# Optimization experiments

Measured on AMD Instinct MI355X. Metric: run time of the kernel, lower is better.

The kernel has to match this reference:

```python
import jax, jax.numpy as jnp
import numpy as np

C = 256
CLS_DIM = 512
GROUPS = C // 4
EPS = 1e-5


def group_norm(x, w, b, groups=GROUPS, eps=EPS):
    # x: [N, C, H, W]
    N, Cc, H, W = x.shape
    xg = x.reshape(N, groups, Cc // groups, H, W)
    mu = xg.mean(axis=(2, 3, 4), keepdims=True)
    var = xg.var(axis=(2, 3, 4), keepdims=True)
    xn = ((xg - mu) * jax.lax.rsqrt(var + eps)).reshape(N, Cc, H, W)
    return xn * w[None, :, None, None] + b[None, :, None, None]


def setup_inputs() -> dict:
    key = jax.random.key(0)
    ks = jax.random.split(key, 12)
    N, H, W = 32, 64, 64
    s = 0.02
    return {
        "X": jax.random.normal(ks[0], (N, C, H, W), jnp.float32),
        "cls": jax.random.normal(ks[1], (N, CLS_DIM), jnp.float32),
        "ln_w": 1.0 + s * jax.random.normal(ks[2], (C,), jnp.float32),
        "ln_b": s * jax.random.normal(ks[3], (C,), jnp.float32),
        "wq": jax.random.normal(ks[4], (C, CLS_DIM), jnp.float32) / np.sqrt(CLS_DIM),
        "bq": s * jax.random.normal(ks[5], (C,), jnp.float32),
        "wk": jax.random.normal(ks[6], (C, CLS_DIM), jnp.float32) / np.sqrt(CLS_DIM),
        "bk": s * jax.random.normal(ks[7], (C,), jnp.float32),
        "conv_w": jax.random.normal(ks[8], (C, C), jnp.float32) / np.sqrt(C),
        "conv_b": s * jax.random.normal(ks[9], (C,), jnp.float32),
        "gn_w": 1.0 + s * jax.random.normal(ks[10], (C,), jnp.float32),
        "gn_b": s * jax.random.normal(ks[11], (C,), jnp.float32),
    }


def reference(X, cls, ln_w, ln_b, wq, bq, wk, bk, conv_w, conv_b, gn_w, gn_b):
    res = X
    Xn = group_norm(X, ln_w, ln_b)
    # NOTE: original code swaps names: K <- Q_emb(cls), Q <- K_emb(cls)
    K = jax.nn.elu(cls @ wq.T + bq) + 1.0              # [N, C]
    Q = (jax.nn.elu(cls @ wk.T + bk) + 1.0) / jnp.sqrt(jnp.float32(C))
    # einsum 'nclw,nco->nolw' with o=1: per-pixel channel contraction with K
    s = jnp.einsum("nchw,nc->nhw", Xn, K)              # [N, H, W]
    # einsum 'nolw,nco->nclw': rank-1 outer product with Q
    X2 = s[:, None, :, :] * Q[:, :, None, None]        # [N, C, H, W]
    # 1x1 conv
    Y = jnp.einsum("nchw,oc->nohw", X2, conv_w) + conv_b[None, :, None, None]
    return group_norm(Y, gn_w, gn_b) + res
```

## Files before the change

### kernel.cpp

```cpp
#include <hip/hip_runtime.h>
#include <math.h>

#define EPSV 1e-5f

typedef float f4v __attribute__((ext_vector_type(4)));

__device__ __forceinline__ float waveReduceSum(float v) {
#pragma unroll
    for (int o = 32; o > 0; o >>= 1) v += __shfl_down(v, o, 64);
    return v;
}

__global__ void k_kq(const float* __restrict__ cls,
                     const float* __restrict__ wq, const float* __restrict__ bq,
                     const float* __restrict__ wk, const float* __restrict__ bk,
                     const float* __restrict__ ln_w,
                     float* __restrict__ Kb, float* __restrict__ Qb,
                     float* __restrict__ Kw) {
    int w = blockIdx.x * 4 + (threadIdx.x >> 6);
    int lane = threadIdx.x & 63;
    int n = w >> 8, c = w & 255;
    const float* cp = cls + (size_t)n * 512;
    const float* qp = wq + (size_t)c * 512;
    const float* kp = wk + (size_t)c * 512;
    float aK = 0.f, aQ = 0.f;
#pragma unroll
    for (int i = 0; i < 8; ++i) {
        int kk = lane + i * 64;
        float cv = cp[kk];
        aK += cv * qp[kk];
        aQ += cv * kp[kk];
    }
    aK = waveReduceSum(aK);
    aQ = waveReduceSum(aQ);
    if (lane == 0) {
        float xk = aK + bq[c];
        float xq = aQ + bk[c];
        float Kv = (xk > 0.f ? xk : expf(xk) - 1.f) + 1.f;
        float Qv = ((xq > 0.f ? xq : expf(xq) - 1.f) + 1.f) * 0.0625f;
        Kb[w] = Kv;
        Qb[w] = Qv;
        Kw[w] = Kv * ln_w[c];
    }
}

__global__ void __launch_bounds__(512) k_pass1(
        const float* __restrict__ X, const float* __restrict__ Kw,
        float* __restrict__ W, float* __restrict__ Sp, float* __restrict__ S2p) {
    int n = blockIdx.x >> 4, tile = blockIdx.x & 15;
    int wv = threadIdx.x >> 6, lane = threadIdx.x & 63;
    __shared__ float kws[256];
    if (threadIdx.x < 256) kws[threadIdx.x] = Kw[n * 256 + threadIdx.x];
    __syncthreads();
    int pix = tile * 256 + lane * 4;
    const float* xb = X + ((size_t)n * 256 << 12) + pix;
#pragma unroll
    for (int go = 0; go < 8; ++go) {
        int g = wv * 8 + go;
        int c0 = g * 4;
        float ax = 0.f, ay = 0.f, az = 0.f, aw = 0.f;
        float s = 0.f, s2 = 0.f;
#pragma unroll
        for (int j = 0; j < 4; ++j) {
            float4 v = *(const float4*)(xb + ((size_t)(c0 + j) << 12));
            float kv = kws[c0 + j];
            ax += kv * v.x; ay += kv * v.y; az += kv * v.z; aw += kv * v.w;
            s  += v.x + v.y + v.z + v.w;
            s2 += v.x * v.x + v.y * v.y + v.z * v.z + v.w * v.w;
        }
        float4 acc = {ax, ay, az, aw};
        *(float4*)(W + ((size_t)(n * 64 + g) << 12) + pix) = acc;
        s = waveReduceSum(s);
        s2 = waveReduceSum(s2);
        if (lane == 0) {
            Sp[blockIdx.x * 64 + g] = s;
            S2p[blockIdx.x * 64 + g] = s2;
        }
    }
}

__global__ void k_s(const float* __restrict__ W,
                    const float* __restrict__ Sp, const float* __restrict__ S2p,
                    const float* __restrict__ Kb, const float* __restrict__ Kw,
                    const float* __restrict__ ln_b,
                    float* __restrict__ sbuf,
                    float* __restrict__ p1, float* __restrict__ p2) {
    int n = blockIdx.x >> 2, tile = blockIdx.x & 3;
    int t = threadIdx.x;
    __shared__ float ivs[64];
    __shared__ float Bsh;
    __shared__ float q1[4], q2[4];
    if (t < 64) {
        float S = 0.f, S2 = 0.f;
#pragma unroll
        for (int tl = 0; tl < 16; ++tl) {
            S  += Sp[(n * 16 + tl) * 64 + t];
            S2 += S2p[(n * 16 + tl) * 64 + t];
        }
        float mu = S * (1.f / 16384.f);
        float var = S2 * (1.f / 16384.f) - mu * mu;
        float iv = rsqrtf(var + EPSV);
        ivs[t] = iv;
        float t1 = 0.f, t2 = 0.f;
#pragma unroll
        for (int j = 0; j < 4; ++j) {
            int c = t * 4 + j;
            t1 += Kb[n * 256 + c] * ln_b[c];
            t2 += Kw[n * 256 + c];
        }
        float r = waveReduceSum(t1 - iv * mu * t2);
        if (t == 0) Bsh = r;
    }
    __syncthreads();
    int pix = tile * 1024 + t * 4;
    const float* wb = W + ((size_t)n * 64 << 12) + pix;
    float Bn = Bsh;
    float sx = Bn, sy = Bn, sz = Bn, sw = Bn;
#pragma unroll 8
    for (int g = 0; g < 64; ++g) {
        float4 v = *(const float4*)(wb + ((size_t)g << 12));
        float iv = ivs[g];
        sx += iv * v.x; sy += iv * v.y; sz += iv * v.z; sw += iv * v.w;
    }
    float4 s4 = {sx, sy, sz, sw};
    *(float4*)(sbuf + n * 4096 + pix) = s4;
    float r1 = waveReduceSum(sx + sy + sz + sw);
    float r2 = waveReduceSum(sx * sx + sy * sy + sz * sz + sw * sw);
    int lane = t & 63, wid = t >> 6;
    if (lane == 0) { q1[wid] = r1; q2[wid] = r2; }
    __syncthreads();
    if (t == 0) {
        p1[blockIdx.x] = q1[0] + q1[1] + q1[2] + q1[3];
        p2[blockIdx.x] = q2[0] + q2[1] + q2[2] + q2[3];
    }
}

__global__ void k_ab(const float* __restrict__ p1, const float* __restrict__ p2,
                     const float* __restrict__ Qb, const float* __restrict__ conv_w,
                     const float* __restrict__ conv_b,
                     const float* __restrict__ gn_w, const float* __restrict__ gn_b,
                     float* __restrict__ alpha, float* __restrict__ beta) {
    int n = blockIdx.x, t = threadIdx.x;
    __shared__ float qs[256];
    __shared__ float rs[256];
    __shared__ float Ms1s, Ms2s;
    qs[t] = Qb[n * 256 + t];
    if (t == 0) {
        float a = 0.f, b = 0.f;
#pragma unroll
        for (int i = 0; i < 4; ++i) { a += p1[n * 4 + i]; b += p2[n * 4 + i]; }
        Ms1s = a * (1.f / 4096.f);
        Ms2s = b * (1.f / 4096.f);
    }
    __syncthreads();
    const float4* cw = (const float4*)(conv_w + (size_t)t * 256);
    const float4* q4 = (const float4*)qs;
    float acc = 0.f;
#pragma unroll 8
    for (int k = 0; k < 64; ++k) {
        float4 w4 = cw[k], v4 = q4[k];
        acc += w4.x * v4.x + w4.y * v4.y + w4.z * v4.z + w4.w * v4.w;
    }
    rs[t] = acc;
    __syncthreads();
    float Ms1 = Ms1s, Ms2 = Ms2s;
    int g = t >> 2;
    float mR = 0.f, mR2 = 0.f, mRb = 0.f, mb = 0.f, mb2 = 0.f;
#pragma unroll
    for (int j = 0; j < 4; ++j) {
        float r = rs[g * 4 + j];
        float bb = conv_b[g * 4 + j];
        mR += r; mR2 += r * r; mRb += r * bb; mb += bb; mb2 += bb * bb;
    }
    mR *= 0.25f; mR2 *= 0.25f; mRb *= 0.25f; mb *= 0.25f; mb2 *= 0.25f;
    float mu = Ms1 * mR + mb;
    float var = Ms2 * mR2 + 2.f * Ms1 * mRb + mb2 - mu * mu;
    float iv = rsqrtf(var + EPSV);
    alpha[n * 256 + t] = acc * iv * gn_w[t];
    beta[n * 256 + t] = (conv_b[t] - mu) * iv * gn_w[t] + gn_b[t];
}

__global__ void k_final(const float* __restrict__ X, const float* __restrict__ sbuf,
                        const float* __restrict__ alpha, const float* __restrict__ beta,
                        float* __restrict__ out) {
    size_t idx4 = (size_t)blockIdx.x * 256 + threadIdx.x;
    size_t e = idx4 * 4;
    int n = (int)(e >> 20);
    int rem = (int)(e & 1048575);
    int o = rem >> 12;
    int pix = rem & 4095;
    float4 x = ((const float4*)X)[idx4];
    float4 s = *(const float4*)(sbuf + n * 4096 + pix);
    float a = alpha[n * 256 + o], b = beta[n * 256 + o];
    f4v r;
    r.x = fmaf(s.x, a, b) + x.x;
    r.y = fmaf(s.y, a, b) + x.y;
    r.z = fmaf(s.z, a, b) + x.z;
    r.w = fmaf(s.w, a, b) + x.w;
    __builtin_nontemporal_store(r, (f4v*)out + idx4);
}

extern "C" void kernel_launch(void* const* d_in, const int* in_sizes, int n_in,
                              void* d_out, int out_size, void* d_ws, size_t ws_size,
                              hipStream_t stream) {
    const float* X      = (const float*)d_in[0];
    const float* cls    = (const float*)d_in[1];
    const float* ln_w   = (const float*)d_in[2];
    const float* ln_b   = (const float*)d_in[3];
    const float* wq     = (const float*)d_in[4];
    const float* bq     = (const float*)d_in[5];
    const float* wk     = (const float*)d_in[6];
    const float* bk     = (const float*)d_in[7];
    const float* conv_w = (const float*)d_in[8];
    const float* conv_b = (const float*)d_in[9];
    const float* gn_w   = (const float*)d_in[10];
    const float* gn_b   = (const float*)d_in[11];

    float* ws = (float*)d_ws;
    float* Kb    = ws;
    float* Qb    = ws + 8192;
    float* Kw    = ws + 16384;
    float* Sp    = ws + 24576;
    float* S2p   = ws + 57344;
    float* p1    = ws + 90112;
    float* p2    = ws + 90240;
    float* alpha = ws + 90368;
    float* beta  = ws + 98560;
    float* sbuf  = ws + 131072;
    float* W     = ws + 262144;

    k_kq<<<2048, 256, 0, stream>>>(cls, wq, bq, wk, bk, ln_w, Kb, Qb, Kw);
    k_pass1<<<512, 512, 0, stream>>>(X, Kw, W, Sp, S2p);
    k_s<<<128, 256, 0, stream>>>(W, Sp, S2p, Kb, Kw, ln_b, sbuf, p1, p2);
    k_ab<<<32, 256, 0, stream>>>(p1, p2, Qb, conv_w, conv_b, gn_w, gn_b, alpha, beta);
    k_final<<<32768, 256, 0, stream>>>(X, sbuf, alpha, beta, (float*)d_out);
}
```

Before: 90.98 us.

## Fuse pass1, score, stats and output into one kernel with per-sample grid barriers

Three kernels (pass1, k_s, k_final) and most of k_ab are merged into one persistent-style kernel of 512 blocks. The per-group K-weighted sums stay in LDS instead of the W workspace buffer, and per-sample statistics are shared through atomic counter spin-barriers across the 16 blocks of each sample. The final residual pass reuses the block's own pixel tile, which removes the W and sbuf global round trips and several launches. This relies on all 16 blocks of a sample being co-resident (512 blocks of 512 threads with about 70KB of LDS each), and spin-waiting carries deadlock and occupancy risk.

```diff
diff --git a/kernel.cpp b/kernel.cpp
--- a/kernel.cpp
+++ b/kernel.cpp
@@ -16,7 +16,8 @@
                      const float* __restrict__ wk, const float* __restrict__ bk,
                      const float* __restrict__ ln_w,
                      float* __restrict__ Kb, float* __restrict__ Qb,
-                     float* __restrict__ Kw) {
+                     float* __restrict__ Kw, unsigned* __restrict__ cnt) {
+    if (blockIdx.x == 0 && threadIdx.x < 64) cnt[threadIdx.x] = 0u;
     int w = blockIdx.x * 4 + (threadIdx.x >> 6);
     int lane = threadIdx.x & 63;
     int n = w >> 8, c = w & 255;
@@ -44,114 +45,11 @@
     }
 }
 
-__global__ void __launch_bounds__(512) k_pass1(
-        const float* __restrict__ X, const float* __restrict__ Kw,
-        float* __restrict__ W, float* __restrict__ Sp, float* __restrict__ S2p) {
-    int n = blockIdx.x >> 4, tile = blockIdx.x & 15;
-    int wv = threadIdx.x >> 6, lane = threadIdx.x & 63;
-    __shared__ float kws[256];
-    if (threadIdx.x < 256) kws[threadIdx.x] = Kw[n * 256 + threadIdx.x];
-    __syncthreads();
-    int pix = tile * 256 + lane * 4;
-    const float* xb = X + ((size_t)n * 256 << 12) + pix;
-#pragma unroll
-    for (int go = 0; go < 8; ++go) {
-        int g = wv * 8 + go;
-        int c0 = g * 4;
-        float ax = 0.f, ay = 0.f, az = 0.f, aw = 0.f;
-        float s = 0.f, s2 = 0.f;
-#pragma unroll
-        for (int j = 0; j < 4; ++j) {
-            float4 v = *(const float4*)(xb + ((size_t)(c0 + j) << 12));
-            float kv = kws[c0 + j];
-            ax += kv * v.x; ay += kv * v.y; az += kv * v.z; aw += kv * v.w;
-            s  += v.x + v.y + v.z + v.w;
-            s2 += v.x * v.x + v.y * v.y + v.z * v.z + v.w * v.w;
-        }
-        float4 acc = {ax, ay, az, aw};
-        *(float4*)(W + ((size_t)(n * 64 + g) << 12) + pix) = acc;
-        s = waveReduceSum(s);
-        s2 = waveReduceSum(s2);
-        if (lane == 0) {
-            Sp[blockIdx.x * 64 + g] = s;
-            S2p[blockIdx.x * 64 + g] = s2;
-        }
-    }
-}
-
-__global__ void k_s(const float* __restrict__ W,
-                    const float* __restrict__ Sp, const float* __restrict__ S2p,
-                    const float* __restrict__ Kb, const float* __restrict__ Kw,
-                    const float* __restrict__ ln_b,
-                    float* __restrict__ sbuf,
-                    float* __restrict__ p1, float* __restrict__ p2) {
-    int n = blockIdx.x >> 2, tile = blockIdx.x & 3;
-    int t = threadIdx.x;
-    __shared__ float ivs[64];
-    __shared__ float Bsh;
-    __shared__ float q1[4], q2[4];
-    if (t < 64) {
-        float S = 0.f, S2 = 0.f;
-#pragma unroll
-        for (int tl = 0; tl < 16; ++tl) {
-            S  += Sp[(n * 16 + tl) * 64 + t];
-            S2 += S2p[(n * 16 + tl) * 64 + t];
-        }
-        float mu = S * (1.f / 16384.f);
-        float var = S2 * (1.f / 16384.f) - mu * mu;
-        float iv = rsqrtf(var + EPSV);
-        ivs[t] = iv;
-        float t1 = 0.f, t2 = 0.f;
-#pragma unroll
-        for (int j = 0; j < 4; ++j) {
-            int c = t * 4 + j;
-            t1 += Kb[n * 256 + c] * ln_b[c];
-            t2 += Kw[n * 256 + c];
-        }
-        float r = waveReduceSum(t1 - iv * mu * t2);
-        if (t == 0) Bsh = r;
-    }
-    __syncthreads();
-    int pix = tile * 1024 + t * 4;
-    const float* wb = W + ((size_t)n * 64 << 12) + pix;
-    float Bn = Bsh;
-    float sx = Bn, sy = Bn, sz = Bn, sw = Bn;
-#pragma unroll 8
-    for (int g = 0; g < 64; ++g) {
-        float4 v = *(const float4*)(wb + ((size_t)g << 12));
-        float iv = ivs[g];
-        sx += iv * v.x; sy += iv * v.y; sz += iv * v.z; sw += iv * v.w;
-    }
-    float4 s4 = {sx, sy, sz, sw};
-    *(float4*)(sbuf + n * 4096 + pix) = s4;
-    float r1 = waveReduceSum(sx + sy + sz + sw);
-    float r2 = waveReduceSum(sx * sx + sy * sy + sz * sz + sw * sw);
-    int lane = t & 63, wid = t >> 6;
-    if (lane == 0) { q1[wid] = r1; q2[wid] = r2; }
-    __syncthreads();
-    if (t == 0) {
-        p1[blockIdx.x] = q1[0] + q1[1] + q1[2] + q1[3];
-        p2[blockIdx.x] = q2[0] + q2[1] + q2[2] + q2[3];
-    }
-}
-
-__global__ void k_ab(const float* __restrict__ p1, const float* __restrict__ p2,
-                     const float* __restrict__ Qb, const float* __restrict__ conv_w,
-                     const float* __restrict__ conv_b,
-                     const float* __restrict__ gn_w, const float* __restrict__ gn_b,
-                     float* __restrict__ alpha, float* __restrict__ beta) {
+__global__ void k_R(const float* __restrict__ Qb, const float* __restrict__ conv_w,
+                    float* __restrict__ R) {
     int n = blockIdx.x, t = threadIdx.x;
     __shared__ float qs[256];
-    __shared__ float rs[256];
-    __shared__ float Ms1s, Ms2s;
     qs[t] = Qb[n * 256 + t];
-    if (t == 0) {
-        float a = 0.f, b = 0.f;
-#pragma unroll
-        for (int i = 0; i < 4; ++i) { a += p1[n * 4 + i]; b += p2[n * 4 + i]; }
-        Ms1s = a * (1.f / 4096.f);
-        Ms2s = b * (1.f / 4096.f);
-    }
     __syncthreads();
     const float4* cw = (const float4*)(conv_w + (size_t)t * 256);
     const float4* q4 = (const float4*)qs;
@@ -161,43 +59,152 @@
         float4 w4 = cw[k], v4 = q4[k];
         acc += w4.x * v4.x + w4.y * v4.y + w4.z * v4.z + w4.w * v4.w;
     }
-    rs[t] = acc;
-    __syncthreads();
-    float Ms1 = Ms1s, Ms2 = Ms2s;
-    int g = t >> 2;
-    float mR = 0.f, mR2 = 0.f, mRb = 0.f, mb = 0.f, mb2 = 0.f;
-#pragma unroll
-    for (int j = 0; j < 4; ++j) {
-        float r = rs[g * 4 + j];
-        float bb = conv_b[g * 4 + j];
-        mR += r; mR2 += r * r; mRb += r * bb; mb += bb; mb2 += bb * bb;
-    }
-    mR *= 0.25f; mR2 *= 0.25f; mRb *= 0.25f; mb *= 0.25f; mb2 *= 0.25f;
-    float mu = Ms1 * mR + mb;
-    float var = Ms2 * mR2 + 2.f * Ms1 * mRb + mb2 - mu * mu;
-    float iv = rsqrtf(var + EPSV);
-    alpha[n * 256 + t] = acc * iv * gn_w[t];
-    beta[n * 256 + t] = (conv_b[t] - mu) * iv * gn_w[t] + gn_b[t];
-}
-
-__global__ void k_final(const float* __restrict__ X, const float* __restrict__ sbuf,
-                        const float* __restrict__ alpha, const float* __restrict__ beta,
-                        float* __restrict__ out) {
-    size_t idx4 = (size_t)blockIdx.x * 256 + threadIdx.x;
-    size_t e = idx4 * 4;
-    int n = (int)(e >> 20);
-    int rem = (int)(e & 1048575);
-    int o = rem >> 12;
-    int pix = rem & 4095;
-    float4 x = ((const float4*)X)[idx4];
-    float4 s = *(const float4*)(sbuf + n * 4096 + pix);
-    float a = alpha[n * 256 + o], b = beta[n * 256 + o];
-    f4v r;
-    r.x = fmaf(s.x, a, b) + x.x;
-    r.y = fmaf(s.y, a, b) + x.y;
-    r.z = fmaf(s.z, a, b) + x.z;
-    r.w = fmaf(s.w, a, b) + x.w;
-    __builtin_nontemporal_store(r, (f4v*)out + idx4);
+    R[n * 256 + t] = acc;
+}
+
+__global__ void __launch_bounds__(512, 4) k_mega(
+        const float* __restrict__ X, const float* __restrict__ Kw,
+        const float* __restrict__ Kb, const float* __restrict__ ln_b,
+        const float* __restrict__ R, const float* __restrict__ conv_b,
+        const float* __restrict__ gn_w, const float* __restrict__ gn_b,
+        float* __restrict__ Sp, float* __restrict__ S2p,
+        float* __restrict__ p1, float* __restrict__ p2,
+        unsigned* __restrict__ cnt1, unsigned* __restrict__ cnt2,
+        float* __restrict__ out) {
+    int bid = blockIdx.x;
+    int n = bid >> 4, tile = bid & 15;
+    int t = threadIdx.x, wv = t >> 6, lane = t & 63;
+
+    __shared__ float kws[256];
+    __shared__ float Wlds[64][256];
+    __shared__ float ivs[64];
+    __shared__ float sS[256];
+    __shared__ float aS[256], bS[256];
+    __shared__ float Rr[256];
+    __shared__ float q1[4], q2[4];
+    __shared__ float Bsh, Ms1s, Ms2s;
+
+    if (t < 256) kws[t] = Kw[n * 256 + t];
+    __syncthreads();
+
+    int pix = tile * 256 + lane * 4;
+    const float* xb = X + ((size_t)n * 256 << 12) + pix;
+
+#pragma unroll
+    for (int go = 0; go < 8; ++go) {
+        int g = wv * 8 + go;
+        int c0 = g * 4;
+        float ax = 0.f, ay = 0.f, az = 0.f, aw = 0.f;
+        float s = 0.f, s2 = 0.f;
+#pragma unroll
+        for (int j = 0; j < 4; ++j) {
+            float4 v = *(const float4*)(xb + ((size_t)(c0 + j) << 12));
+            float kv = kws[c0 + j];
+            ax += kv * v.x; ay += kv * v.y; az += kv * v.z; aw += kv * v.w;
+            s  += v.x + v.y + v.z + v.w;
+            s2 += v.x * v.x + v.y * v.y + v.z * v.z + v.w * v.w;
+        }
+        float4 acc = {ax, ay, az, aw};
+        *(float4*)(&Wlds[g][lane * 4]) = acc;
+        s = waveReduceSum(s);
+        s2 = waveReduceSum(s2);
+        if (lane == 0) {
+            Sp[bid * 64 + g] = s;
+            S2p[bid * 64 + g] = s2;
+        }
+    }
+    __threadfence();
+    __syncthreads();
+    if (t == 0) {
+        atomicAdd(&cnt1[n], 1u);
+        while (atomicAdd(&cnt1[n], 0u) < 16u) __builtin_amdgcn_s_sleep(8);
+    }
+    __syncthreads();
+
+    if (t < 64) {
+        float S = 0.f, S2 = 0.f;
+#pragma unroll
+        for (int tl = 0; tl < 16; ++tl) {
+            S  += Sp[(n * 16 + tl) * 64 + t];
+            S2 += S2p[(n * 16 + tl) * 64 + t];
+        }
+        float mu = S * (1.f / 16384.f);
+        float var = S2 * (1.f / 16384.f) - mu * mu;
+        float iv = rsqrtf(var + EPSV);
+        ivs[t] = iv;
+        float t1 = 0.f, t2 = 0.f;
+#pragma unroll
+        for (int j = 0; j < 4; ++j) {
+            int c = t * 4 + j;
+            t1 += Kb[n * 256 + c] * ln_b[c];
+            t2 += kws[c];
+        }
+        float r = waveReduceSum(t1 - iv * mu * t2);
+        if (t == 0) Bsh = r;
+    }
+    __syncthreads();
+
+    if (t < 256) {
+        float s = Bsh;
+#pragma unroll 16
+        for (int g = 0; g < 64; ++g) s += ivs[g] * Wlds[g][t];
+        sS[t] = s;
+        float r1 = waveReduceSum(s);
+        float r2 = waveReduceSum(s * s);
+        if (lane == 0) { q1[wv] = r1; q2[wv] = r2; }
+    }
+    __syncthreads();
+    if (t == 0) {
+        p1[bid] = q1[0] + q1[1] + q1[2] + q1[3];
+        p2[bid] = q2[0] + q2[1] + q2[2] + q2[3];
+        __threadfence();
+        atomicAdd(&cnt2[n], 1u);
+        while (atomicAdd(&cnt2[n], 0u) < 16u) __builtin_amdgcn_s_sleep(8);
+    }
+    __syncthreads();
+
+    if (t == 0) {
+        float a = 0.f, b = 0.f;
+#pragma unroll
+        for (int tl = 0; tl < 16; ++tl) { a += p1[n * 16 + tl]; b += p2[n * 16 + tl]; }
+        Ms1s = a * (1.f / 4096.f);
+        Ms2s = b * (1.f / 4096.f);
+    }
+    if (t < 256) Rr[t] = R[n * 256 + t];
+    __syncthreads();
+    if (t < 256) {
+        int g4 = (t >> 2) << 2;
+        float mR = 0.f, mR2 = 0.f, mRb = 0.f, mb = 0.f, mb2 = 0.f;
+#pragma unroll
+        for (int j = 0; j < 4; ++j) {
+            float r = Rr[g4 + j];
+            float bb = conv_b[g4 + j];
+            mR += r; mR2 += r * r; mRb += r * bb; mb += bb; mb2 += bb * bb;
+        }
+        mR *= 0.25f; mR2 *= 0.25f; mRb *= 0.25f; mb *= 0.25f; mb2 *= 0.25f;
+        float mu = Ms1s * mR + mb;
+        float var = Ms2s * mR2 + 2.f * Ms1s * mRb + mb2 - mu * mu;
+        float iv = rsqrtf(var + EPSV);
+        aS[t] = Rr[t] * iv * gn_w[t];
+        bS[t] = (conv_b[t] - mu) * iv * gn_w[t] + gn_b[t];
+    }
+    __syncthreads();
+
+    float4 s4 = *(const float4*)(&sS[lane * 4]);
+    const float* xo = X + ((size_t)n * 256 << 12) + pix;
+    float* oo = out + ((size_t)n * 256 << 12) + pix;
+#pragma unroll 4
+    for (int j = 0; j < 32; ++j) {
+        int o = wv * 32 + j;
+        float4 x = *(const float4*)(xo + ((size_t)o << 12));
+        float a = aS[o], b = bS[o];
+        f4v r;
+        r.x = fmaf(s4.x, a, b) + x.x;
+        r.y = fmaf(s4.y, a, b) + x.y;
+        r.z = fmaf(s4.z, a, b) + x.z;
+        r.w = fmaf(s4.w, a, b) + x.w;
+        __builtin_nontemporal_store(r, (f4v*)(oo + ((size_t)o << 12)));
+    }
 }
 
 extern "C" void kernel_launch(void* const* d_in, const int* in_sizes, int n_in,
@@ -217,21 +224,19 @@
     const float* gn_b   = (const float*)d_in[11];
 
     float* ws = (float*)d_ws;
-    float* Kb    = ws;
-    float* Qb    = ws + 8192;
-    float* Kw    = ws + 16384;
-    float* Sp    = ws + 24576;
-    float* S2p   = ws + 57344;
-    float* p1    = ws + 90112;
-    float* p2    = ws + 90240;
-    float* alpha = ws + 90368;
-    float* beta  = ws + 98560;
-    float* sbuf  = ws + 131072;
-    float* W     = ws + 262144;
-
-    k_kq<<<2048, 256, 0, stream>>>(cls, wq, bq, wk, bk, ln_w, Kb, Qb, Kw);
-    k_pass1<<<512, 512, 0, stream>>>(X, Kw, W, Sp, S2p);
-    k_s<<<128, 256, 0, stream>>>(W, Sp, S2p, Kb, Kw, ln_b, sbuf, p1, p2);
-    k_ab<<<32, 256, 0, stream>>>(p1, p2, Qb, conv_w, conv_b, gn_w, gn_b, alpha, beta);
-    k_final<<<32768, 256, 0, stream>>>(X, sbuf, alpha, beta, (float*)d_out);
-}
+    float* Kb   = ws;
+    float* Qb   = ws + 8192;
+    float* Kw   = ws + 16384;
+    float* R    = ws + 24576;
+    float* Sp   = ws + 32768;
+    float* S2p  = ws + 65536;
+    float* p1   = ws + 98304;
+    float* p2   = ws + 98816;
+    unsigned* cnt = (unsigned*)(ws + 99328);
+
+    k_kq<<<2048, 256, 0, stream>>>(cls, wq, bq, wk, bk, ln_w, Kb, Qb, Kw, cnt);
+    k_R<<<32, 256, 0, stream>>>(Qb, conv_w, R);
+    k_mega<<<512, 512, 0, stream>>>(X, Kw, Kb, ln_b, R, conv_b, gn_w, gn_b,
+                                    Sp, S2p, p1, p2, cnt, cnt + 32,
+                                    (float*)d_out);
+}
```

Result: slower. 228.8 us (+151.5%).

## Fold alpha/beta kernel into k_s and k_final, double k_s grid

Applied to the files above, without the earlier changes.

Removes the separate k_ab launch. The conv_w·Q matvec moves into tile-0 blocks of k_s, and the per-channel GroupNorm alpha/beta are recomputed per block inside k_final from p1/p2/R. k_s now uses 8 tiles per sample with float2 loads, giving 256 blocks for better occupancy. The cost is redundant scalar work in each of the 32768 final blocks, plus a longer tail for the tile-0 blocks of k_s.

```diff
diff --git a/kernel.cpp b/kernel.cpp
--- a/kernel.cpp
+++ b/kernel.cpp
@@ -83,13 +83,16 @@
                     const float* __restrict__ Sp, const float* __restrict__ S2p,
                     const float* __restrict__ Kb, const float* __restrict__ Kw,
                     const float* __restrict__ ln_b,
+                    const float* __restrict__ Qb, const float* __restrict__ conv_w,
                     float* __restrict__ sbuf,
-                    float* __restrict__ p1, float* __restrict__ p2) {
-    int n = blockIdx.x >> 2, tile = blockIdx.x & 3;
+                    float* __restrict__ p1, float* __restrict__ p2,
+                    float* __restrict__ R) {
+    int n = blockIdx.x >> 3, tile = blockIdx.x & 7;
     int t = threadIdx.x;
     __shared__ float ivs[64];
     __shared__ float Bsh;
     __shared__ float q1[4], q2[4];
+    __shared__ float qs[256];
     if (t < 64) {
         float S = 0.f, S2 = 0.f;
 #pragma unroll
@@ -112,20 +115,20 @@
         if (t == 0) Bsh = r;
     }
     __syncthreads();
-    int pix = tile * 1024 + t * 4;
+    int pix = tile * 512 + t * 2;
     const float* wb = W + ((size_t)n * 64 << 12) + pix;
     float Bn = Bsh;
-    float sx = Bn, sy = Bn, sz = Bn, sw = Bn;
-#pragma unroll 8
+    float sx = Bn, sy = Bn;
+#pragma unroll 16
     for (int g = 0; g < 64; ++g) {
-        float4 v = *(const float4*)(wb + ((size_t)g << 12));
+        float2 v = *(const float2*)(wb + ((size_t)g << 12));
         float iv = ivs[g];
-        sx += iv * v.x; sy += iv * v.y; sz += iv * v.z; sw += iv * v.w;
-    }
-    float4 s4 = {sx, sy, sz, sw};
-    *(float4*)(sbuf + n * 4096 + pix) = s4;
-    float r1 = waveReduceSum(sx + sy + sz + sw);
-    float r2 = waveReduceSum(sx * sx + sy * sy + sz * sz + sw * sw);
+        sx += iv * v.x; sy += iv * v.y;
+    }
+    float2 s2v = {sx, sy};
+    *(float2*)(sbuf + n * 4096 + pix) = s2v;
+    float r1 = waveReduceSum(sx + sy);
+    float r2 = waveReduceSum(sx * sx + sy * sy);
     int lane = t & 63, wid = t >> 6;
     if (lane == 0) { q1[wid] = r1; q2[wid] = r2; }
     __syncthreads();
@@ -133,65 +136,57 @@
         p1[blockIdx.x] = q1[0] + q1[1] + q1[2] + q1[3];
         p2[blockIdx.x] = q2[0] + q2[1] + q2[2] + q2[3];
     }
-}
-
-__global__ void k_ab(const float* __restrict__ p1, const float* __restrict__ p2,
-                     const float* __restrict__ Qb, const float* __restrict__ conv_w,
-                     const float* __restrict__ conv_b,
-                     const float* __restrict__ gn_w, const float* __restrict__ gn_b,
-                     float* __restrict__ alpha, float* __restrict__ beta) {
-    int n = blockIdx.x, t = threadIdx.x;
-    __shared__ float qs[256];
-    __shared__ float rs[256];
-    __shared__ float Ms1s, Ms2s;
-    qs[t] = Qb[n * 256 + t];
-    if (t == 0) {
-        float a = 0.f, b = 0.f;
-#pragma unroll
-        for (int i = 0; i < 4; ++i) { a += p1[n * 4 + i]; b += p2[n * 4 + i]; }
-        Ms1s = a * (1.f / 4096.f);
-        Ms2s = b * (1.f / 4096.f);
-    }
-    __syncthreads();
-    const float4* cw = (const float4*)(conv_w + (size_t)t * 256);
-    const float4* q4 = (const float4*)qs;
-    float acc = 0.f;
+    if (tile == 0) {
+        qs[t] = Qb[n * 256 + t];
+        __syncthreads();
+        const float4* cw = (const float4*)(conv_w + (size_t)t * 256);
+        const float4* q4 = (const float4*)qs;
+        float acc = 0.f;
 #pragma unroll 8
-    for (int k = 0; k < 64; ++k) {
-        float4 w4 = cw[k], v4 = q4[k];
-        acc += w4.x * v4.x + w4.y * v4.y + w4.z * v4.z + w4.w * v4.w;
-    }
-    rs[t] = acc;
-    __syncthreads();
-    float Ms1 = Ms1s, Ms2 = Ms2s;
-    int g = t >> 2;
+        for (int k = 0; k < 64; ++k) {
+            float4 w4 = cw[k], v4 = q4[k];
+            acc += w4.x * v4.x + w4.y * v4.y + w4.z * v4.z + w4.w * v4.w;
+        }
+        R[n * 256 + t] = acc;
+    }
+}
+
+__global__ void __launch_bounds__(256) k_final(
+        const float* __restrict__ X, const float* __restrict__ sbuf,
+        const float* __restrict__ p1, const float* __restrict__ p2,
+        const float* __restrict__ R, const float* __restrict__ conv_b,
+        const float* __restrict__ gn_w, const float* __restrict__ gn_b,
+        float* __restrict__ out) {
+    size_t idx4 = (size_t)blockIdx.x * 256 + threadIdx.x;
+    size_t e0 = (size_t)blockIdx.x * 1024;
+    int n = (int)(e0 >> 20);
+    int o = (int)((e0 & 1048575) >> 12);
+
+    float a1 = 0.f, a2 = 0.f;
+#pragma unroll
+    for (int i = 0; i < 8; ++i) { a1 += p1[n * 8 + i]; a2 += p2[n * 8 + i]; }
+    float Ms1 = a1 * (1.f / 4096.f);
+    float Ms2 = a2 * (1.f / 4096.f);
+    int g4 = o & ~3;
     float mR = 0.f, mR2 = 0.f, mRb = 0.f, mb = 0.f, mb2 = 0.f;
 #pragma unroll
     for (int j = 0; j < 4; ++j) {
-        float r = rs[g * 4 + j];
-        float bb = conv_b[g * 4 + j];
+        float r = R[n * 256 + g4 + j];
+        float bb = conv_b[g4 + j];
         mR += r; mR2 += r * r; mRb += r * bb; mb += bb; mb2 += bb * bb;
     }
     mR *= 0.25f; mR2 *= 0.25f; mRb *= 0.25f; mb *= 0.25f; mb2 *= 0.25f;
     float mu = Ms1 * mR + mb;
     float var = Ms2 * mR2 + 2.f * Ms1 * mRb + mb2 - mu * mu;
     float iv = rsqrtf(var + EPSV);
-    alpha[n * 256 + t] = acc * iv * gn_w[t];
-    beta[n * 256 + t] = (conv_b[t] - mu) * iv * gn_w[t] + gn_b[t];
-}
-
-__global__ void k_final(const float* __restrict__ X, const float* __restrict__ sbuf,
-                        const float* __restrict__ alpha, const float* __restrict__ beta,
-                        float* __restrict__ out) {
-    size_t idx4 = (size_t)blockIdx.x * 256 + threadIdx.x;
+    float gw = gn_w[o];
+    float a = R[n * 256 + o] * iv * gw;
+    float b = (conv_b[o] - mu) * iv * gw + gn_b[o];
+
     size_t e = idx4 * 4;
-    int n = (int)(e >> 20);
-    int rem = (int)(e & 1048575);
-    int o = rem >> 12;
-    int pix = rem & 4095;
+    int pix = (int)(e & 4095);
     float4 x = ((const float4*)X)[idx4];
     float4 s = *(const float4*)(sbuf + n * 4096 + pix);
-    float a = alpha[n * 256 + o], b = beta[n * 256 + o];
     f4v r;
     r.x = fmaf(s.x, a, b) + x.x;
     r.y = fmaf(s.y, a, b) + x.y;
@@ -223,15 +218,15 @@
     float* Sp    = ws + 24576;
     float* S2p   = ws + 57344;
     float* p1    = ws + 90112;
-    float* p2    = ws + 90240;
-    float* alpha = ws + 90368;
-    float* beta  = ws + 98560;
+    float* p2    = ws + 90368;
+    float* R     = ws + 90624;
     float* sbuf  = ws + 131072;
     float* W     = ws + 262144;
 
     k_kq<<<2048, 256, 0, stream>>>(cls, wq, bq, wk, bk, ln_w, Kb, Qb, Kw);
     k_pass1<<<512, 512, 0, stream>>>(X, Kw, W, Sp, S2p);
-    k_s<<<128, 256, 0, stream>>>(W, Sp, S2p, Kb, Kw, ln_b, sbuf, p1, p2);
-    k_ab<<<32, 256, 0, stream>>>(p1, p2, Qb, conv_w, conv_b, gn_w, gn_b, alpha, beta);
-    k_final<<<32768, 256, 0, stream>>>(X, sbuf, alpha, beta, (float*)d_out);
-}
+    k_s<<<256, 256, 0, stream>>>(W, Sp, S2p, Kb, Kw, ln_b, Qb, conv_w,
+                                 sbuf, p1, p2, R);
+    k_final<<<32768, 256, 0, stream>>>(X, sbuf, p1, p2, R, conv_b, gn_w, gn_b,
+                                       (float*)d_out);
+}
```

Result: no change. 91.96 us (+1.1%).
